# Kernel tuning notes

Hardware: AMD Instinct MI355X
Metric: run time of the kernel (lower is better)

## Reference

```python
import jax, jax.numpy as jnp
import numpy as np

B, N = 32, 1024  # batch, square grid size (Ny == Nx forced by expand_as in the torch module)


def setup_inputs() -> dict:
    key = jax.random.key(0)
    k1, k2, k3 = jax.random.split(key, 3)
    xaxis = jnp.arange(N, dtype=jnp.float32)            # sorted knot positions along x
    yaxis = jnp.arange(N, dtype=jnp.float32)            # sorted knot positions along y
    signal = jax.random.normal(k1, (B, N, N), dtype=jnp.float32)
    # queries constrained to [0.5, N-3] so gathered indices I+1 stay in-bounds for the
    # (N-1)-length slope tensors, matching the valid-domain assumption of the torch code
    xs = jax.random.uniform(k2, (N,), minval=0.5, maxval=float(N - 3), dtype=jnp.float32)
    ys = jax.random.uniform(k3, (N,), minval=0.5, maxval=float(N - 3), dtype=jnp.float32)
    return {"xaxis": xaxis, "yaxis": yaxis, "signal": signal, "xs": xs, "ys": ys}


def _h_poly(t):
    # Cubic Hermite basis: rows of A = [[1,0,-3,2],[0,1,-2,1],[0,0,3,-2],[0,0,-1,1]] dotted with [1,t,t^2,t^3]
    t2 = t * t
    t3 = t2 * t
    h0 = 1.0 - 3.0 * t2 + 2.0 * t3
    h1 = t - 2.0 * t2 + t3
    h2 = 3.0 * t2 - 2.0 * t3
    h3 = t3 - t2
    return h0, h1, h2, h3


def _interp1d(inp, axis1d, m, q):
    # inp: [..., N] values, m: [..., N-1] slopes, axis1d: [N] shared knots, q: [M] queries
    # torch.searchsorted(x0[...,1:-1], xs) with right=False == jnp.searchsorted side='left'
    I = jnp.searchsorted(axis1d[1:-1], q)          # [M], int
    x = axis1d[I]                                  # [M]
    dx = axis1d[I + 1] - x                         # [M]
    t = (q - x) / dx                               # [M]
    h0, h1, h2, h3 = _h_poly(t)

    def g(a, idx):
        idx_b = jnp.broadcast_to(idx, a.shape[:-1] + idx.shape)
        return jnp.take_along_axis(a, idx_b, axis=-1)

    return (h0 * g(inp, I)
            + h1 * g(m, I) * dx
            + h2 * g(inp, I + 1)
            + h3 * g(m, I + 1) * dx)


def reference(xaxis, yaxis, signal, xs, ys):
    # slopes (x1/x2 are just the 1D axes broadcast over signal, so diffs reduce to 1D diffs)
    m1 = (signal[..., 1:] - signal[..., :-1]) / (xaxis[1:] - xaxis[:-1])        # [B,N,N-1]
    sT = jnp.swapaxes(signal, -2, -1)
    m2 = (sT[..., 1:] - sT[..., :-1]) / (yaxis[1:] - yaxis[:-1])                # [B,N,N-1]
    out = jnp.swapaxes(_interp1d(signal, xaxis, m1, xs), -2, -1)                # [B,Mx,N]
    out = jnp.swapaxes(_interp1d(out, yaxis, m2, ys), -2, -1)                   # [B,My,N]
    return out
```

## Files before the change

kernel.cpp:

```cpp
#include <hip/hip_runtime.h>


#define NGRID 1024
#define BATCH 32

__global__ __launch_bounds__(256) void hermite2d_fused(
    const float* __restrict__ signal,
    const float* __restrict__ xs,
    const float* __restrict__ ys,
    float* __restrict__ out)
{
    const int k = blockIdx.x;
    const int b = blockIdx.y;

    __shared__ float row0[NGRID];
    __shared__ float row1[NGRID];
    __shared__ float row2[NGRID];

    const float qy = ys[k];
    int Iy = (int)floorf(qy);
    if (Iy < 0) Iy = 0;
    if (Iy > NGRID - 3) Iy = NGRID - 3;
    const float ty  = qy - (float)Iy;
    const float ty2 = ty * ty;
    const float ty3 = ty2 * ty;
    const float h0y = 1.0f - 3.0f * ty2 + 2.0f * ty3;
    const float h1y = ty - 2.0f * ty2 + ty3;
    const float h2y = 3.0f * ty2 - 2.0f * ty3;
    const float h3y = ty3 - ty2;

    const float4* src4 = (const float4*)(signal + ((size_t)b * NGRID + (size_t)Iy) * NGRID);
    float4* r0 = (float4*)row0;
    float4* r1 = (float4*)row1;
    float4* r2 = (float4*)row2;
    const int nv = NGRID / 4;
    {
        const int i = threadIdx.x;
        r0[i] = src4[i];
        r1[i] = src4[i + nv];
        r2[i] = src4[i + 2 * nv];
    }
    __syncthreads();

    float* orow = out + ((size_t)b * NGRID + (size_t)k) * NGRID;

    #pragma unroll
    for (int pp = 0; pp < NGRID / 256; ++pp) {
        const int p = threadIdx.x + pp * 256;

        const float qx = xs[p];
        int Ix = (int)floorf(qx);
        if (Ix < 0) Ix = 0;
        if (Ix > NGRID - 3) Ix = NGRID - 3;
        const float tx = qx - (float)Ix;
        const float t2 = tx * tx;
        const float t3 = t2 * tx;
        const float h0 = 1.0f - 3.0f * t2 + 2.0f * t3;
        const float h1 = tx - 2.0f * t2 + t3;
        const float h2 = 3.0f * t2 - 2.0f * t3;
        const float h3 = t3 - t2;

        const float a0 = row0[Ix], a1 = row0[Ix + 1], a2 = row0[Ix + 2];
        const float u0 = h0 * a0 + h1 * (a1 - a0) + h2 * a1 + h3 * (a2 - a1);
        const float b0 = row1[Ix], b1 = row1[Ix + 1], b2 = row1[Ix + 2];
        const float u1 = h0 * b0 + h1 * (b1 - b0) + h2 * b1 + h3 * (b2 - b1);

        const float s0 = row0[p], s1 = row1[p], s2 = row2[p];
        orow[p] = h0y * u0 + h1y * (s1 - s0) + h2y * u1 + h3y * (s2 - s1);
    }
}

extern "C" void kernel_launch(void* const* d_in, const int* in_sizes, int n_in,
                              void* d_out, int out_size, void* d_ws, size_t ws_size,
                              hipStream_t stream) {
    const float* signal = (const float*)d_in[2];
    const float* xs     = (const float*)d_in[3];
    const float* ys     = (const float*)d_in[4];
    float* out          = (float*)d_out;

    dim3 grid(NGRID, BATCH);
    hermite2d_fused<<<grid, 256, 0, stream>>>(signal, xs, ys, out);
}
```

Before: 246.6 us.

## Precombine y-weighted rows in shared memory and vectorize per-thread outputs

```diff
diff --git a/kernel.cpp b/kernel.cpp
--- a/kernel.cpp
+++ b/kernel.cpp
@@ -12,10 +12,9 @@
 {
     const int k = blockIdx.x;
     const int b = blockIdx.y;
+    const int t = threadIdx.x;
 
-    __shared__ float row0[NGRID];
-    __shared__ float row1[NGRID];
-    __shared__ float row2[NGRID];
+    __shared__ float crow[NGRID];
 
     const float qy = ys[k];
     int Iy = (int)floorf(qy);
@@ -30,44 +29,50 @@
     const float h3y = ty3 - ty2;
 
     const float4* src4 = (const float4*)(signal + ((size_t)b * NGRID + (size_t)Iy) * NGRID);
-    float4* r0 = (float4*)row0;
-    float4* r1 = (float4*)row1;
-    float4* r2 = (float4*)row2;
-    const int nv = NGRID / 4;
-    {
-        const int i = threadIdx.x;
-        r0[i] = src4[i];
-        r1[i] = src4[i + nv];
-        r2[i] = src4[i + 2 * nv];
-    }
+    const float4 r0 = src4[t];
+    const float4 r1 = src4[t + NGRID / 4];
+    const float4 r2 = src4[t + NGRID / 2];
+
+    float4 c;
+    c.x = h0y * r0.x + h2y * r1.x;
+    c.y = h0y * r0.y + h2y * r1.y;
+    c.z = h0y * r0.z + h2y * r1.z;
+    c.w = h0y * r0.w + h2y * r1.w;
+    ((float4*)crow)[t] = c;
+
+    float colp[4];
+    colp[0] = h1y * (r1.x - r0.x) + h3y * (r2.x - r1.x);
+    colp[1] = h1y * (r1.y - r0.y) + h3y * (r2.y - r1.y);
+    colp[2] = h1y * (r1.z - r0.z) + h3y * (r2.z - r1.z);
+    colp[3] = h1y * (r1.w - r0.w) + h3y * (r2.w - r1.w);
+
+    const float4 q4 = ((const float4*)xs)[t];
+    const float qx[4] = { q4.x, q4.y, q4.z, q4.w };
+
     __syncthreads();
 
-    float* orow = out + ((size_t)b * NGRID + (size_t)k) * NGRID;
-
+    float4 res;
+    float* resp = (float*)&res;
     #pragma unroll
-    for (int pp = 0; pp < NGRID / 256; ++pp) {
-        const int p = threadIdx.x + pp * 256;
-
-        const float qx = xs[p];
-        int Ix = (int)floorf(qx);
+    for (int j = 0; j < 4; ++j) {
+        const float q = qx[j];
+        int Ix = (int)floorf(q);
         if (Ix < 0) Ix = 0;
         if (Ix > NGRID - 3) Ix = NGRID - 3;
-        const float tx = qx - (float)Ix;
+        const float tx = q - (float)Ix;
         const float t2 = tx * tx;
         const float t3 = t2 * tx;
-        const float h0 = 1.0f - 3.0f * t2 + 2.0f * t3;
-        const float h1 = tx - 2.0f * t2 + t3;
-        const float h2 = 3.0f * t2 - 2.0f * t3;
-        const float h3 = t3 - t2;
+        const float w0 = 1.0f - tx - t2 + t3;
+        const float w1 = tx + 2.0f * (t2 - t3);
+        const float w2 = t3 - t2;
+        const float c0 = crow[Ix];
+        const float c1 = crow[Ix + 1];
+        const float c2 = crow[Ix + 2];
+        resp[j] = w0 * c0 + w1 * c1 + w2 * c2 + colp[j];
+    }
 
-        const float a0 = row0[Ix], a1 = row0[Ix + 1], a2 = row0[Ix + 2];
-        const float u0 = h0 * a0 + h1 * (a1 - a0) + h2 * a1 + h3 * (a2 - a1);
-        const float b0 = row1[Ix], b1 = row1[Ix + 1], b2 = row1[Ix + 2];
-        const float u1 = h0 * b0 + h1 * (b1 - b0) + h2 * b1 + h3 * (b2 - b1);
-
-        const float s0 = row0[p], s1 = row1[p], s2 = row2[p];
-        orow[p] = h0y * u0 + h1y * (s1 - s0) + h2y * u1 + h3y * (s2 - s1);
-    }
+    float4* orow4 = (float4*)(out + ((size_t)b * NGRID + (size_t)k) * NGRID);
+    orow4[t] = res;
 }
 
 extern "C" void kernel_launch(void* const* d_in, const int* in_sizes, int n_in,
```

After: 239.3 us. -3.0%, faster.
